# Optimization experiments

Hardware: AMD Instinct MI355X
Metric: run time of the kernel (lower is better)

The kernel has to match this reference:

```python
import jax, jax.numpy as jnp
import numpy as np
from math import sqrt

B, P, D = 4, 2048, 1024
H, DK = 16, 64  # n_heads, d_keys


def setup_inputs() -> dict:
    key = jax.random.key(0)
    ks = jax.random.split(key, 6)
    s = 1.0 / sqrt(D)
    return {
        "target_embedding": jax.random.normal(ks[0], (B, P, D), dtype=jnp.float32),
        "Wq": jax.random.normal(ks[1], (D, H * DK), dtype=jnp.float32) * s,
        "bq": jnp.zeros((H * DK,), dtype=jnp.float32),
        "Wk": jax.random.normal(ks[2], (D, H * DK), dtype=jnp.float32) * s,
        "bk": jnp.zeros((H * DK,), dtype=jnp.float32),
        "Wv": jax.random.normal(ks[3], (D, H * DK), dtype=jnp.float32) * s,
        "bv": jnp.zeros((H * DK,), dtype=jnp.float32),
        "Wo": jax.random.normal(ks[4], (H * DK, D), dtype=jnp.float32) * s,
        "bo": jnp.zeros((D,), dtype=jnp.float32),
    }


def reference(target_embedding, Wq, bq, Wk, bk, Wv, bv, Wo, bo):
    x = target_embedding
    b, p, _ = x.shape
    # QKV projections -> [B, P, H, DK]
    q = (x @ Wq + bq).reshape(b, p, H, DK)
    k = (x @ Wk + bk).reshape(b, p, H, DK)
    v = (x @ Wv + bv).reshape(b, p, H, DK)
    scale = 1.0 / sqrt(DK)
    scores = jnp.einsum("bphd,bqhd->bhpq", q, k)  # [B, H, P, P]
    A = jax.nn.softmax(scale * scores, axis=-1)  # dropout is identity in eval
    rep = jnp.einsum("bhpq,bqhd->bphd", A, v).reshape(b, p, H * DK)
    return rep @ Wo + bo
```

## Files before the change

kernel.cpp:

```cpp
#include <hip/hip_runtime.h>

typedef __attribute__((ext_vector_type(8))) short short8;
typedef __attribute__((ext_vector_type(4))) short short4v;
typedef __attribute__((ext_vector_type(4))) float f32x4;
typedef __attribute__((ext_vector_type(4))) unsigned short ushort4v;
typedef __attribute__((ext_vector_type(2))) unsigned int uint2v;

#define GLOBAL_AS __attribute__((address_space(1)))
#define LDS_AS    __attribute__((address_space(3)))

__device__ __forceinline__ unsigned short f2bf(float f) {
    unsigned int u = __float_as_uint(f);
    u += 0x7fffu + ((u >> 16) & 1u);
    return (unsigned short)(u >> 16);
}

__device__ __forceinline__ unsigned int pack_rhu(float a, float b) {
    unsigned int ua = __float_as_uint(a) + 0x8000u;
    unsigned int ub = __float_as_uint(b) + 0x8000u;
    return __builtin_amdgcn_perm(ub, ua, 0x07060302u);
}

__device__ __forceinline__ short4v pack4_rhu(float p0, float p1, float p2, float p3) {
    uint2v uu;
    uu[0] = pack_rhu(p0, p1);
    uu[1] = pack_rhu(p2, p3);
    return __builtin_bit_cast(short4v, uu);
}

__device__ __forceinline__ float fexp2(float x) {
    return __builtin_amdgcn_exp2f(x);
}

__device__ __forceinline__ void async_cp16(void* lds, const void* g) {
    __builtin_amdgcn_global_load_lds((GLOBAL_AS unsigned int*)g,
                                     (LDS_AS unsigned int*)lds, 16, 0, 0);
}

#define SCL2E 0.18033688011112042591999058512524f

__global__ void prep_kernel(const float* __restrict__ X,
                            const float* __restrict__ Wq,
                            const float* __restrict__ Wk,
                            const float* __restrict__ Wv,
                            const float* __restrict__ Wo,
                            unsigned short* __restrict__ Xb,
                            unsigned short* __restrict__ Wts) {
    const int z = blockIdx.z;
    if (z < 4) {
        __shared__ float tile[32][33];
        const float* src = (z == 0) ? Wq : (z == 1) ? Wk : (z == 2) ? Wv : Wo;
        unsigned short* dst = Wts + z * 1048576;
        const int tx = threadIdx.x, ty = threadIdx.y;
        const int x0 = blockIdx.x * 32, y0 = blockIdx.y * 32;
#pragma unroll
        for (int i = 0; i < 32; i += 8)
            tile[ty + i][tx] = src[(y0 + ty + i) * 1024 + x0 + tx];
        __syncthreads();
#pragma unroll
        for (int i = 0; i < 32; i += 8)
            dst[(x0 + ty + i) * 1024 + y0 + tx] = f2bf(tile[tx][ty + i]);
    } else {
        const int tid = threadIdx.y * 32 + threadIdx.x;
        const int chunk = blockIdx.y * 32 + blockIdx.x;
        const int base = chunk * 8192;
#pragma unroll
        for (int pass = 0; pass < 8; ++pass) {
            int i = base + pass * 1024 + tid * 4;
            float4 v = *(const float4*)&X[i];
            ushort4v o;
            o.x = f2bf(v.x); o.y = f2bf(v.y); o.z = f2bf(v.z); o.w = f2bf(v.w);
            *(ushort4v*)&Xb[i] = o;
        }
    }
}

__device__ __forceinline__ void gemm_stage_tile(
    const unsigned short* __restrict__ A, const unsigned short* __restrict__ Bt,
    int m0, int n0, int k0, int tid, unsigned short* Asb, unsigned short* Bsb) {
#pragma unroll
    for (int i = 0; i < 2; ++i) {
        int s = tid + 256 * i;
        int r = s >> 2, gp = s & 3;
        int g = gp ^ ((r >> 1) & 3);
        async_cp16(&Asb[s * 8], &A[(m0 + r) * 1024 + k0 + g * 8]);
        async_cp16(&Bsb[s * 8], &Bt[(n0 + r) * 1024 + k0 + g * 8]);
    }
}

__device__ __forceinline__ void gemm_mainloop_128(
    const unsigned short* __restrict__ A, const unsigned short* __restrict__ Bt,
    int m0, int n0, unsigned short* GS, f32x4 acc[4][4]) {
    const int tid = threadIdx.x;
    const int lane = tid & 63;
    const int wave = tid >> 6;
    const int wr = wave >> 1, wc = wave & 1;
    const int c = lane & 15, quad = lane >> 4;
    unsigned short* As = GS;
    unsigned short* Bs = GS + 8192;

#pragma unroll
    for (int mt = 0; mt < 4; ++mt)
#pragma unroll
        for (int nt = 0; nt < 4; ++nt)
            acc[mt][nt] = (f32x4)0.0f;

    gemm_stage_tile(A, Bt, m0, n0, 0, tid, As, Bs);

    for (int k0 = 0; k0 < 1024; k0 += 32) {
        const int cur = (k0 >> 5) & 1;
        unsigned short* Asb = As + cur * 4096;
        unsigned short* Bsb = Bs + cur * 4096;
        asm volatile("s_waitcnt vmcnt(0)" ::: "memory");
        __syncthreads();
        if (k0 + 32 < 1024)
            gemm_stage_tile(A, Bt, m0, n0, k0 + 32, tid,
                            As + (cur ^ 1) * 4096, Bs + (cur ^ 1) * 4096);

        short8 af[4], bf[4];
#pragma unroll
        for (int mt = 0; mt < 4; ++mt) {
            int r = wr * 64 + mt * 16 + c;
            int gp = quad ^ ((r >> 1) & 3);
            af[mt] = *(const short8*)&Asb[r * 32 + gp * 8];
        }
#pragma unroll
        for (int nt = 0; nt < 4; ++nt) {
            int r = wc * 64 + nt * 16 + c;
            int gp = quad ^ ((r >> 1) & 3);
            bf[nt] = *(const short8*)&Bsb[r * 32 + gp * 8];
        }
#pragma unroll
        for (int mt = 0; mt < 4; ++mt)
#pragma unroll
            for (int nt = 0; nt < 4; ++nt)
                acc[mt][nt] = __builtin_amdgcn_mfma_f32_16x16x32_bf16(
                    af[mt], bf[nt], acc[mt][nt], 0, 0, 0);
    }
}

__global__ __launch_bounds__(256, 4) void gemm_qkv_kernel(
    const unsigned short* __restrict__ Xb, const unsigned short* __restrict__ Wts,
    const float* __restrict__ bq, const float* __restrict__ bk,
    const float* __restrict__ bv, unsigned short* __restrict__ Qb,
    unsigned short* __restrict__ Kb, unsigned short* __restrict__ Vtb) {
    __shared__ __align__(16) unsigned short GS[17408];
    const int z = blockIdx.z;
    const unsigned short* Wz = Wts + z * 1048576;
    const int m0 = blockIdx.x * 128;
    const int n0 = blockIdx.y * 128;
    f32x4 acc[4][4];
    gemm_mainloop_128(Wz, Xb, m0, n0, GS, acc);

    const int lane = threadIdx.x & 63, wave = threadIdx.x >> 6;
    const int wr = wave >> 1, wc = wave & 1;
    const int c = lane & 15, quad = lane >> 4;

    if (z < 2) {
        const float* bias = (z == 0) ? bq : bk;
        unsigned short* dst = (z == 0) ? Qb : Kb;
        const float qs = (z == 0) ? SCL2E : 1.0f;
        __syncthreads();
        unsigned short* TILE = GS;
#pragma unroll
        for (int mt = 0; mt < 4; ++mt) {
            int ocb = m0 + wr * 64 + mt * 16 + quad * 4;
            float b0 = bias[ocb + 0], b1 = bias[ocb + 1];
            float b2 = bias[ocb + 2], b3 = bias[ocb + 3];
#pragma unroll
            for (int nt = 0; nt < 4; ++nt) {
                int pl = wc * 64 + nt * 16 + c;
                int dkl = wr * 64 + mt * 16 + quad * 4;
                short4v frag = pack4_rhu((acc[mt][nt][0] + b0) * qs,
                                         (acc[mt][nt][1] + b1) * qs,
                                         (acc[mt][nt][2] + b2) * qs,
                                         (acc[mt][nt][3] + b3) * qs);
                *(short4v*)&TILE[pl * 136 + dkl] = frag;
            }
        }
        __syncthreads();
        const int hbase = m0 >> 6;
#pragma unroll
        for (int pass = 0; pass < 32; ++pass) {
            int pl = pass * 4 + (lane >> 4);
            int dkl8 = (lane & 15) * 8;
            short8 v = *(const short8*)&TILE[pl * 136 + dkl8];
            int pp = n0 + pl;
            int b = pp >> 11, p = pp & 2047;
            int h = hbase + (dkl8 >> 6), dk = dkl8 & 63;
            *(short8*)&dst[((b * 16 + h) * 2048 + p) * 64 + dk] = v;
        }
    } else {
        float bb2[4][4];
#pragma unroll
        for (int mt = 0; mt < 4; ++mt)
#pragma unroll
            for (int r = 0; r < 4; ++r)
                bb2[mt][r] = bv[m0 + wr * 64 + mt * 16 + quad * 4 + r];
#pragma unroll
        for (int nt = 0; nt < 4; ++nt) {
            int colp = n0 + wc * 64 + nt * 16 + c;
            int b = colp >> 11, p = colp & 2047;
#pragma unroll
            for (int mt = 0; mt < 4; ++mt) {
#pragma unroll
                for (int r = 0; r < 4; ++r) {
                    int rowv = m0 + wr * 64 + mt * 16 + quad * 4 + r;
                    int h = rowv >> 6, dk = rowv & 63;
                    float v = acc[mt][nt][r] + bb2[mt][r];
                    Vtb[(b * 16 + h) * 131072 + dk * 2048 + p] = f2bf(v);
                }
            }
        }
    }
}

__device__ __forceinline__ void load_kv_regs(
    const unsigned short* __restrict__ Kbh, const unsigned short* __restrict__ Vbh,
    int k0, int tid, short8 kr[2], short8 vr[2]) {
#pragma unroll
    for (int i = 0; i < 2; ++i) {
        int s = tid + 256 * i;
        int r = s >> 3, gp = s & 7;
        int g = gp ^ (r & 7);
        kr[i] = *(const short8*)&Kbh[(k0 + r) * 64 + g * 8];
        vr[i] = *(const short8*)&Vbh[r * 2048 + k0 + gp * 8];
    }
}

__global__ __launch_bounds__(256, 2) void attn_kernel(
    const unsigned short* __restrict__ Q, const unsigned short* __restrict__ K,
    const unsigned short* __restrict__ Vt, unsigned short* __restrict__ rep) {
    __shared__ __align__(16) unsigned short SMEM[17408];
    const int tid = threadIdx.x, lane = tid & 63, wave = tid >> 6;
    const int c = lane & 15, quad = lane >> 4;
    const int bh = blockIdx.y;
    const int q0 = blockIdx.x * 256 + wave * 64;
    const unsigned short* Qbh = Q + bh * (2048 * 64);
    const unsigned short* Kbh = K + bh * (2048 * 64);
    const unsigned short* Vbh = Vt + bh * (64 * 2048);

    short8 qf[4][2];
#pragma unroll
    for (int t = 0; t < 4; ++t)
#pragma unroll
        for (int ks = 0; ks < 2; ++ks)
            qf[t][ks] = *(const short8*)&Qbh[(q0 + t * 16 + c) * 64 + ks * 32 + quad * 8];

    short8 kr[2], vr[2];
    load_kv_regs(Kbh, Vbh, 0, tid, kr, vr);

    f32x4 o[4][4];
    float lpart[4] = {0.0f, 0.0f, 0.0f, 0.0f};
#pragma unroll
    for (int t = 0; t < 4; ++t)
#pragma unroll
        for (int d = 0; d < 4; ++d) o[t][d] = (f32x4)0.0f;

    for (int it = 0; it < 32; ++it) {
        const int buf = it & 1;
        unsigned short* Ksb = &SMEM[buf * 4096];
        unsigned short* Vsb = &SMEM[8192 + buf * 4608];
#pragma unroll
        for (int i = 0; i < 2; ++i) {
            int s = tid + 256 * i;
            int r = s >> 3, gp = s & 7;
            *(short8*)&Ksb[s * 8] = kr[i];
            *(short8*)&Vsb[r * 72 + gp * 8] = vr[i];
        }
        __syncthreads();
        if (it < 31)
            load_kv_regs(Kbh, Vbh, (it + 1) * 64, tid, kr, vr);

        short8 kf[4][2];
#pragma unroll
        for (int nt = 0; nt < 4; ++nt)
#pragma unroll
            for (int ks = 0; ks < 2; ++ks) {
                int r = nt * 16 + c;
                int gp2 = (quad + 4 * ks) ^ (r & 7);
                kf[nt][ks] = *(const short8*)&Ksb[r * 64 + gp2 * 8];
            }

        short4v vf[4][4];
#pragma unroll
        for (int dkt = 0; dkt < 4; ++dkt) {
            int r = dkt * 16 + c;
#pragma unroll
            for (int kt = 0; kt < 4; ++kt)
                vf[dkt][kt] = *(const short4v*)&Vsb[r * 72 + kt * 16 + quad * 4];
        }

        f32x4 zc = (f32x4)0.0f;
        zc = __builtin_amdgcn_mfma_f32_16x16x32_bf16(kf[0][0], qf[0][0], zc, 0, 0, 0);
        zc = __builtin_amdgcn_mfma_f32_16x16x32_bf16(kf[0][1], qf[0][1], zc, 0, 0, 0);
#pragma unroll
        for (int u = 0; u < 16; ++u) {
            const int t = u >> 2, nt = u & 3;
            f32x4 zn = (f32x4)0.0f;
            if (u < 15) {
                const int t2 = (u + 1) >> 2, nt2 = (u + 1) & 3;
                zn = __builtin_amdgcn_mfma_f32_16x16x32_bf16(kf[nt2][0], qf[t2][0], zn, 0, 0, 0);
                zn = __builtin_amdgcn_mfma_f32_16x16x32_bf16(kf[nt2][1], qf[t2][1], zn, 0, 0, 0);
            }
            float p0 = fexp2(zc[0]), p1 = fexp2(zc[1]);
            float p2 = fexp2(zc[2]), p3 = fexp2(zc[3]);
            lpart[t] += (p0 + p1) + (p2 + p3);
            short4v pf = pack4_rhu(p0, p1, p2, p3);
#pragma unroll
            for (int dkt = 0; dkt < 4; ++dkt)
                o[t][dkt] = __builtin_amdgcn_mfma_f32_16x16x16bf16_1k(
                    vf[dkt][nt], pf, o[t][dkt], 0, 0, 0);
            zc = zn;
        }
    }

    float inv[4];
#pragma unroll
    for (int t = 0; t < 4; ++t) {
        float l = lpart[t];
        l += __shfl_xor(l, 16);
        l += __shfl_xor(l, 32);
        inv[t] = 1.0f / l;
    }

    __syncthreads();
    const int b = bh >> 4, h = bh & 15;
    unsigned short* ob = &SMEM[wave * 2304];
#pragma unroll
    for (int pass = 0; pass < 2; ++pass) {
#pragma unroll
        for (int th = 0; th < 2; ++th) {
            int t = pass * 2 + th;
#pragma unroll
            for (int dkt = 0; dkt < 4; ++dkt) {
                short4v frag = pack4_rhu(o[t][dkt][0] * inv[t], o[t][dkt][1] * inv[t],
                                         o[t][dkt][2] * inv[t], o[t][dkt][3] * inv[t]);
                *(short4v*)&ob[(th * 16 + c) * 72 + dkt * 16 + quad * 4] = frag;
            }
        }
        asm volatile("s_waitcnt lgkmcnt(0)" ::: "memory");
#pragma unroll
        for (int sp = 0; sp < 4; ++sp) {
            int qr = sp * 8 + (lane >> 3);
            int d8 = (lane & 7) * 8;
            short8 row = *(const short8*)&ob[qr * 72 + d8];
            *(short8*)&rep[(b * 2048 + q0 + pass * 32 + qr) * 1024 + h * 64 + d8] = row;
        }
    }
}

__device__ __forceinline__ void gemm_out_stage_tile(
    const unsigned short* __restrict__ A, const unsigned short* __restrict__ Bt,
    int m0, int n0, int k0, int tid, unsigned short* Asb, unsigned short* Bsb) {
#pragma unroll
    for (int i = 0; i < 2; ++i) {
        int s = tid + 256 * i;
        int r = s >> 2, gp = s & 3;
        int g = gp ^ ((r >> 1) & 3);
        async_cp16(&Asb[s * 8], &A[(m0 + r) * 1024 + k0 + g * 8]);
    }
    {
        int s = tid;
        int r = s >> 2, gp = s & 3;
        int g = gp ^ ((r >> 1) & 3);
        async_cp16(&Bsb[s * 8], &Bt[(n0 + r) * 1024 + k0 + g * 8]);
    }
}

__global__ __launch_bounds__(256, 4) void gemm_out_kernel(
    const unsigned short* __restrict__ rep, const unsigned short* __restrict__ Wot,
    const float* __restrict__ bo, float* __restrict__ out) {
    __shared__ __align__(16) unsigned short GS[12288];
    const int tid = threadIdx.x;
    const int lane = tid & 63;
    const int wave = tid >> 6;
    const int wr = wave >> 1, wc = wave & 1;
    const int c = lane & 15, quad = lane >> 4;
    const int m0 = blockIdx.y * 128, n0 = blockIdx.x * 64;
    unsigned short* As = GS;
    unsigned short* Bs = GS + 8192;

    f32x4 acc[4][2];
#pragma unroll
    for (int mt = 0; mt < 4; ++mt)
#pragma unroll
        for (int nt = 0; nt < 2; ++nt)
            acc[mt][nt] = (f32x4)0.0f;

    gemm_out_stage_tile(rep, Wot, m0, n0, 0, tid, As, Bs);

    for (int k0 = 0; k0 < 1024; k0 += 32) {
        const int cur = (k0 >> 5) & 1;
        unsigned short* Asb = As + cur * 4096;
        unsigned short* Bsb = Bs + cur * 2048;
        asm volatile("s_waitcnt vmcnt(0)" ::: "memory");
        __syncthreads();
        if (k0 + 32 < 1024)
            gemm_out_stage_tile(rep, Wot, m0, n0, k0 + 32, tid,
                                As + (cur ^ 1) * 4096, Bs + (cur ^ 1) * 2048);

        short8 af[4], bf[2];
#pragma unroll
        for (int mt = 0; mt < 4; ++mt) {
            int r = wr * 64 + mt * 16 + c;
            int gp = quad ^ ((r >> 1) & 3);
            af[mt] = *(const short8*)&Asb[r * 32 + gp * 8];
        }
#pragma unroll
        for (int nt = 0; nt < 2; ++nt) {
            int r = wc * 32 + nt * 16 + c;
            int gp = quad ^ ((r >> 1) & 3);
            bf[nt] = *(const short8*)&Bsb[r * 32 + gp * 8];
        }
#pragma unroll
        for (int mt = 0; mt < 4; ++mt)
#pragma unroll
            for (int nt = 0; nt < 2; ++nt)
                acc[mt][nt] = __builtin_amdgcn_mfma_f32_16x16x32_bf16(
                    af[mt], bf[nt], acc[mt][nt], 0, 0, 0);
    }

#pragma unroll
    for (int nt = 0; nt < 2; ++nt) {
        int col = n0 + wc * 32 + nt * 16 + c;
        float bb = bo[col];
#pragma unroll
        for (int mt = 0; mt < 4; ++mt) {
            int row = m0 + wr * 64 + mt * 16 + quad * 4;
#pragma unroll
            for (int r = 0; r < 4; ++r)
                out[(row + r) * 1024 + col] = acc[mt][nt][r] + bb;
        }
    }
}

extern "C" void kernel_launch(void* const* d_in, const int* in_sizes, int n_in,
                              void* d_out, int out_size, void* d_ws, size_t ws_size,
                              hipStream_t stream) {
    (void)in_sizes; (void)n_in; (void)out_size; (void)ws_size;
    const float* X  = (const float*)d_in[0];
    const float* Wq = (const float*)d_in[1];
    const float* bq = (const float*)d_in[2];
    const float* Wk = (const float*)d_in[3];
    const float* bk = (const float*)d_in[4];
    const float* Wv = (const float*)d_in[5];
    const float* bv = (const float*)d_in[6];
    const float* Wo = (const float*)d_in[7];
    const float* bo = (const float*)d_in[8];
    float* out = (float*)d_out;

    char* ws = (char*)d_ws;
    unsigned short* Xb   = (unsigned short*)(ws);
    unsigned short* Wts  = (unsigned short*)(ws + (16u << 20));
    unsigned short* Qb   = (unsigned short*)(ws + (24u << 20));
    unsigned short* Kb   = (unsigned short*)(ws + (40u << 20));
    unsigned short* Vtb  = (unsigned short*)(ws + (56u << 20));
    unsigned short* repb = (unsigned short*)(ws);

    prep_kernel<<<dim3(32, 32, 5), dim3(32, 8), 0, stream>>>(X, Wq, Wk, Wv, Wo, Xb, Wts);
    gemm_qkv_kernel<<<dim3(8, 64, 3), 256, 0, stream>>>(Xb, Wts, bq, bk, bv, Qb, Kb, Vtb);
    attn_kernel<<<dim3(8, 64), 256, 0, stream>>>(Qb, Kb, Vtb, repb);
    gemm_out_kernel<<<dim3(16, 64), 256, 0, stream>>>(repb, Wts + 3 * 1048576, bo, out);
}
```

Before: 296.0 us.

## Split attention KV tiles across wave pairs with async LDS staging

The attention kernel now has each pair of waves share one 64-query slice and split every 64-key tile into halves. The two partial outputs and row sums are then reduced through LDS. Each block covers 128 queries instead of 256, which doubles the grid, and the launch bound rises to 3 blocks per CU. K/V tiles are now copied straight into swizzled LDS with async copies instead of passing through registers, removing register staging and the padded V layout. In exchange, the kernel adds a cross-wave reduction with extra barriers, and half the waves sit idle during the epilogue.

```diff
diff --git a/kernel.cpp b/kernel.cpp
--- a/kernel.cpp
+++ b/kernel.cpp
@@ -215,27 +215,28 @@
     }
 }
 
-__device__ __forceinline__ void load_kv_regs(
+__device__ __forceinline__ void stage_kv_async(
     const unsigned short* __restrict__ Kbh, const unsigned short* __restrict__ Vbh,
-    int k0, int tid, short8 kr[2], short8 vr[2]) {
+    int k0, int tid, unsigned short* Ksb, unsigned short* Vsb) {
 #pragma unroll
     for (int i = 0; i < 2; ++i) {
         int s = tid + 256 * i;
         int r = s >> 3, gp = s & 7;
         int g = gp ^ (r & 7);
-        kr[i] = *(const short8*)&Kbh[(k0 + r) * 64 + g * 8];
-        vr[i] = *(const short8*)&Vbh[r * 2048 + k0 + gp * 8];
-    }
-}
-
-__global__ __launch_bounds__(256, 2) void attn_kernel(
+        async_cp16(&Ksb[s * 8], &Kbh[(k0 + r) * 64 + g * 8]);
+        async_cp16(&Vsb[s * 8], &Vbh[r * 2048 + k0 + g * 8]);
+    }
+}
+
+__global__ __launch_bounds__(256, 3) void attn_kernel(
     const unsigned short* __restrict__ Q, const unsigned short* __restrict__ K,
     const unsigned short* __restrict__ Vt, unsigned short* __restrict__ rep) {
-    __shared__ __align__(16) unsigned short SMEM[17408];
+    __shared__ __align__(16) unsigned short SMEM[16384];
     const int tid = threadIdx.x, lane = tid & 63, wave = tid >> 6;
     const int c = lane & 15, quad = lane >> 4;
+    const int wq = wave & 1, wk = wave >> 1;
     const int bh = blockIdx.y;
-    const int q0 = blockIdx.x * 256 + wave * 64;
+    const int q0 = blockIdx.x * 128 + wq * 64;
     const unsigned short* Qbh = Q + bh * (2048 * 64);
     const unsigned short* Kbh = K + bh * (2048 * 64);
     const unsigned short* Vbh = Vt + bh * (64 * 2048);
@@ -247,8 +248,7 @@
         for (int ks = 0; ks < 2; ++ks)
             qf[t][ks] = *(const short8*)&Qbh[(q0 + t * 16 + c) * 64 + ks * 32 + quad * 8];
 
-    short8 kr[2], vr[2];
-    load_kv_regs(Kbh, Vbh, 0, tid, kr, vr);
+    stage_kv_async(Kbh, Vbh, 0, tid, &SMEM[0], &SMEM[8192]);
 
     f32x4 o[4][4];
     float lpart[4] = {0.0f, 0.0f, 0.0f, 0.0f};
@@ -260,71 +260,92 @@
     for (int it = 0; it < 32; ++it) {
         const int buf = it & 1;
         unsigned short* Ksb = &SMEM[buf * 4096];
-        unsigned short* Vsb = &SMEM[8192 + buf * 4608];
-#pragma unroll
-        for (int i = 0; i < 2; ++i) {
-            int s = tid + 256 * i;
-            int r = s >> 3, gp = s & 7;
-            *(short8*)&Ksb[s * 8] = kr[i];
-            *(short8*)&Vsb[r * 72 + gp * 8] = vr[i];
-        }
+        unsigned short* Vsb = &SMEM[8192 + buf * 4096];
+        asm volatile("s_waitcnt vmcnt(0)" ::: "memory");
         __syncthreads();
         if (it < 31)
-            load_kv_regs(Kbh, Vbh, (it + 1) * 64, tid, kr, vr);
-
-        short8 kf[4][2];
-#pragma unroll
-        for (int nt = 0; nt < 4; ++nt)
-#pragma unroll
-            for (int ks = 0; ks < 2; ++ks) {
-                int r = nt * 16 + c;
-                int gp2 = (quad + 4 * ks) ^ (r & 7);
-                kf[nt][ks] = *(const short8*)&Ksb[r * 64 + gp2 * 8];
-            }
-
-        short4v vf[4][4];
-#pragma unroll
-        for (int dkt = 0; dkt < 4; ++dkt) {
-            int r = dkt * 16 + c;
-#pragma unroll
-            for (int kt = 0; kt < 4; ++kt)
-                vf[dkt][kt] = *(const short4v*)&Vsb[r * 72 + kt * 16 + quad * 4];
-        }
-
-        f32x4 zc = (f32x4)0.0f;
-        zc = __builtin_amdgcn_mfma_f32_16x16x32_bf16(kf[0][0], qf[0][0], zc, 0, 0, 0);
-        zc = __builtin_amdgcn_mfma_f32_16x16x32_bf16(kf[0][1], qf[0][1], zc, 0, 0, 0);
-#pragma unroll
-        for (int u = 0; u < 16; ++u) {
-            const int t = u >> 2, nt = u & 3;
-            f32x4 zn = (f32x4)0.0f;
-            if (u < 15) {
-                const int t2 = (u + 1) >> 2, nt2 = (u + 1) & 3;
-                zn = __builtin_amdgcn_mfma_f32_16x16x32_bf16(kf[nt2][0], qf[t2][0], zn, 0, 0, 0);
-                zn = __builtin_amdgcn_mfma_f32_16x16x32_bf16(kf[nt2][1], qf[t2][1], zn, 0, 0, 0);
-            }
-            float p0 = fexp2(zc[0]), p1 = fexp2(zc[1]);
-            float p2 = fexp2(zc[2]), p3 = fexp2(zc[3]);
-            lpart[t] += (p0 + p1) + (p2 + p3);
-            short4v pf = pack4_rhu(p0, p1, p2, p3);
-#pragma unroll
-            for (int dkt = 0; dkt < 4; ++dkt)
-                o[t][dkt] = __builtin_amdgcn_mfma_f32_16x16x16bf16_1k(
-                    vf[dkt][nt], pf, o[t][dkt], 0, 0, 0);
-            zc = zn;
-        }
-    }
+            stage_kv_async(Kbh, Vbh, (it + 1) * 64, tid,
+                           &SMEM[(buf ^ 1) * 4096], &SMEM[8192 + (buf ^ 1) * 4096]);
+
+#pragma unroll
+        for (int nt = 0; nt < 2; ++nt) {
+            short8 kf0, kf1;
+            {
+                int r = wk * 32 + nt * 16 + c;
+                kf0 = *(const short8*)&Ksb[r * 64 + ((quad) ^ (r & 7)) * 8];
+                kf1 = *(const short8*)&Ksb[r * 64 + ((quad + 4) ^ (r & 7)) * 8];
+            }
+            short4v vf[4];
+            const int ktg = wk * 2 + nt;
+#pragma unroll
+            for (int dkt = 0; dkt < 4; ++dkt) {
+                int r = dkt * 16 + c;
+                int g = (2 * ktg + (quad >> 1)) ^ (r & 7);
+                vf[dkt] = *(const short4v*)&Vsb[r * 64 + g * 8 + (quad & 1) * 4];
+            }
+#pragma unroll
+            for (int t = 0; t < 4; ++t) {
+                f32x4 z4 = (f32x4)0.0f;
+                z4 = __builtin_amdgcn_mfma_f32_16x16x32_bf16(kf0, qf[t][0], z4, 0, 0, 0);
+                z4 = __builtin_amdgcn_mfma_f32_16x16x32_bf16(kf1, qf[t][1], z4, 0, 0, 0);
+                float p0 = fexp2(z4[0]), p1 = fexp2(z4[1]);
+                float p2 = fexp2(z4[2]), p3 = fexp2(z4[3]);
+                lpart[t] += (p0 + p1) + (p2 + p3);
+                short4v pf = pack4_rhu(p0, p1, p2, p3);
+#pragma unroll
+                for (int dkt = 0; dkt < 4; ++dkt)
+                    o[t][dkt] = __builtin_amdgcn_mfma_f32_16x16x16bf16_1k(
+                        vf[dkt], pf, o[t][dkt], 0, 0, 0);
+            }
+        }
+    }
+
+#pragma unroll
+    for (int t = 0; t < 4; ++t) {
+        lpart[t] += __shfl_xor(lpart[t], 16);
+        lpart[t] += __shfl_xor(lpart[t], 32);
+    }
+
+    float* FS = (float*)SMEM;
+    __syncthreads();
+#pragma unroll
+    for (int p = 0; p < 2; ++p) {
+        if (wk == 1) {
+#pragma unroll
+            for (int tt = 0; tt < 2; ++tt)
+#pragma unroll
+                for (int dkt = 0; dkt < 4; ++dkt) {
+                    int off = (tt * 16 + dkt * 4) ^ ((lane & 7) << 2);
+                    *(f32x4*)&FS[wq * 2048 + lane * 32 + off] = o[p * 2 + tt][dkt];
+                }
+            if (p == 0 && quad == 0) {
+#pragma unroll
+                for (int t = 0; t < 4; ++t) FS[4096 + wq * 64 + t * 16 + c] = lpart[t];
+            }
+        }
+        __syncthreads();
+        if (wk == 0) {
+#pragma unroll
+            for (int tt = 0; tt < 2; ++tt)
+#pragma unroll
+                for (int dkt = 0; dkt < 4; ++dkt) {
+                    int off = (tt * 16 + dkt * 4) ^ ((lane & 7) << 2);
+                    f32x4 v = *(const f32x4*)&FS[wq * 2048 + lane * 32 + off];
+                    o[p * 2 + tt][dkt] += v;
+                }
+            if (p == 0) {
+#pragma unroll
+                for (int t = 0; t < 4; ++t) lpart[t] += FS[4096 + wq * 64 + t * 16 + c];
+            }
+        }
+        __syncthreads();
+    }
+    if (wk != 0) return;
 
     float inv[4];
 #pragma unroll
-    for (int t = 0; t < 4; ++t) {
-        float l = lpart[t];
-        l += __shfl_xor(l, 16);
-        l += __shfl_xor(l, 32);
-        inv[t] = 1.0f / l;
-    }
-
-    __syncthreads();
+    for (int t = 0; t < 4; ++t) inv[t] = 1.0f / lpart[t];
+
     const int b = bh >> 4, h = bh & 15;
     unsigned short* ob = &SMEM[wave * 2304];
 #pragma unroll
@@ -460,6 +481,6 @@
 
     prep_kernel<<<dim3(32, 32, 5), dim3(32, 8), 0, stream>>>(X, Wq, Wk, Wv, Wo, Xb, Wts);
     gemm_qkv_kernel<<<dim3(8, 64, 3), 256, 0, stream>>>(Xb, Wts, bq, bk, bv, Qb, Kb, Vtb);
-    attn_kernel<<<dim3(8, 64), 256, 0, stream>>>(Qb, Kb, Vtb, repb);
+    attn_kernel<<<dim3(16, 64), 256, 0, stream>>>(Qb, Kb, Vtb, repb);
     gemm_out_kernel<<<dim3(16, 64), 256, 0, stream>>>(repb, Wts + 3 * 1048576, bo, out);
 }
```

Result: no change. 296.0 us (+0.0%).
